# Optimization experiments

Measured on AMD Instinct MI355X. Metric: run time of the kernel, lower is better.

Reference implementation:

```python
import jax, jax.numpy as jnp
import numpy as np

B, M, D, H, FF = 2, 2048, 1024, 16, 2624
DH = D // H  # 64, power of 2 as required by the kernel
EPS = 1e-5
THETA = 10000.0


def setup_inputs() -> dict:
    key = jax.random.key(0)
    ks = jax.random.split(key, 12)
    hidden_states = jax.random.normal(ks[0], (B, M, D), dtype=jnp.float32)
    # padding mask: 1=valid, 0=pad; vary valid lengths per batch element
    lengths = jnp.array([M, 3 * M // 4], dtype=jnp.int32)
    attention_mask = (jnp.arange(M)[None, :] < lengths[:, None]).astype(jnp.int32)
    s = 0.02
    return {
        "hidden_states": hidden_states,
        "attention_mask": attention_mask,
        "ln1_w": jnp.ones((D,), jnp.float32),
        "ln1_b": jnp.zeros((D,), jnp.float32),
        "wqkv_w": s * jax.random.normal(ks[1], (3 * D, D), jnp.float32),
        "wqkv_b": jnp.zeros((3 * D,), jnp.float32),
        "wo_w": s * jax.random.normal(ks[2], (D, D), jnp.float32),
        "ln2_w": jnp.ones((D,), jnp.float32),
        "ln2_b": jnp.zeros((D,), jnp.float32),
        "wi_w": s * jax.random.normal(ks[3], (2 * FF, D), jnp.float32),
        "wo_mlp_w": s * jax.random.normal(ks[4], (D, FF), jnp.float32),
    }


def _layernorm(x, w, b):
    mu = jnp.mean(x, axis=-1, keepdims=True)
    var = jnp.mean(jnp.square(x - mu), axis=-1, keepdims=True)
    return (x - mu) * jax.lax.rsqrt(var + EPS) * w + b


def _rope(q, k):
    # q,k: [B,H,M,DH]; half-split RoPE (q1' = q1*c - q2*s; q2' = q1*s + q2*c)
    half = DH // 2
    inv_freq = 1.0 / (THETA ** (jnp.arange(0, DH, 2, dtype=jnp.float32) / DH))  # [half]
    freqs = jnp.arange(M, dtype=jnp.float32)[:, None] * inv_freq[None, :]      # [M, half]
    c = jnp.cos(freqs)[None, None]  # [1,1,M,half]
    s = jnp.sin(freqs)[None, None]
    q1, q2 = q[..., :half], q[..., half:]
    k1, k2 = k[..., :half], k[..., half:]
    q = jnp.concatenate([q1 * c - q2 * s, q1 * s + q2 * c], axis=-1)
    k = jnp.concatenate([k1 * c - k2 * s, k1 * s + k2 * c], axis=-1)
    return q, k


def reference(hidden_states, attention_mask, ln1_w, ln1_b, wqkv_w, wqkv_b,
              wo_w, ln2_w, ln2_b, wi_w, wo_mlp_w):
    x = hidden_states
    xn = _layernorm(x, ln1_w, ln1_b)
    qkv = (xn @ wqkv_w.T + wqkv_b).reshape(B, M, 3, H, DH)
    q, k, v = [jnp.transpose(qkv[:, :, i], (0, 2, 1, 3)) for i in range(3)]  # [B,H,M,DH]
    q, k = _rope(q, k)
    scale = 1.0 / np.sqrt(DH)
    scores = jnp.einsum("bhmd,bhnd->bhmn", q, k) * scale
    keep = (attention_mask > 0)[:, None, None, :]  # [B,1,1,M] key-padding mask
    scores = jnp.where(keep, scores, -jnp.inf)
    attn = jax.nn.softmax(scores, axis=-1)
    o = jnp.einsum("bhmn,bhnd->bhmd", attn, v)
    attn_out = jnp.transpose(o, (0, 2, 1, 3)).reshape(B, M, D)
    x = x + attn_out @ wo_w.T
    # ModernBERT GeGLU MLP
    h = _layernorm(x, ln2_w, ln2_b)
    g = h @ wi_w.T
    inp, gate = g[..., :FF], g[..., FF:]
    x = x + (jax.nn.gelu(inp, approximate=False) * gate) @ wo_mlp_w.T
    return x
```

## Files before the change

### kernel.cpp

```cpp
#include <hip/hip_runtime.h>
#include <hip/hip_bf16.h>
#include <math.h>

#define BB 2
#define MM 2048
#define DD 1024
#define HH 16
#define DHH 64
#define FF_ 2624
#define FFP 2688
#define TT (BB*MM)

typedef unsigned short u16;
typedef __attribute__((ext_vector_type(4))) unsigned short ushort4v;
typedef __attribute__((ext_vector_type(8))) short short8;
typedef __attribute__((ext_vector_type(4))) float floatx4;
typedef __attribute__((ext_vector_type(16))) float floatx16;

#define SCALE2 0.18033688011112043f

#define WAITVM(N) asm volatile("s_waitcnt vmcnt(" #N ")" ::: "memory")
#define CFENCE()  asm volatile("" ::: "memory")

__device__ __forceinline__ u16 f2bf(float f) {
    __hip_bfloat16 h = __float2bfloat16(f);
    return *(u16*)&h;
}
__device__ __forceinline__ float bf2f(u16 u) {
    __hip_bfloat16 h; *(u16*)&h = u;
    return __bfloat162float(h);
}
__device__ __forceinline__ float gelu_exact(float x) {
    return 0.5f * x * (1.0f + erff(x * 0.70710678118654752f));
}
__device__ __forceinline__ void gload_lds16(const void* g, void* l) {
    __builtin_amdgcn_global_load_lds(
        (const __attribute__((address_space(1))) unsigned int*)g,
        (__attribute__((address_space(3))) unsigned int*)l, 16, 0, 0);
}
__device__ __forceinline__ unsigned int cvt_pk_bf16(float a, float b) {
    unsigned int r;
    asm("v_cvt_pk_bf16_f32 %0, %1, %2" : "=v"(r) : "v"(a), "v"(b));
    return r;
}
__device__ __forceinline__ short8 pack8(float a0, float a1, float a2, float a3,
                                        float a4, float a5, float a6, float a7) {
    union { unsigned int u[4]; short8 s; } r;
    r.u[0] = cvt_pk_bf16(a0, a1); r.u[1] = cvt_pk_bf16(a2, a3);
    r.u[2] = cvt_pk_bf16(a4, a5); r.u[3] = cvt_pk_bf16(a6, a7);
    return r.s;
}

__device__ __forceinline__ int xcd_swizzle(int id, int nb) {
    if (nb & 7) return id;
    return (id & 7) * (nb >> 3) + (id >> 3);
}

__global__ void cvt_all(const float* __restrict__ wqkv, const float* __restrict__ wo,
                        const float* __restrict__ wi, const float* __restrict__ womlp,
                        u16* __restrict__ dqkv, u16* __restrict__ dwo,
                        u16* __restrict__ dinp, u16* __restrict__ dgate,
                        u16* __restrict__ dmlp, float2* __restrict__ tab) {
    int bid = blockIdx.x, tid = threadIdx.x;
    if (bid < 3072) {
        int i = (bid * 256 + tid) * 4;
        float4 v = *(const float4*)(wqkv + i);
        ushort4v o = {f2bf(v.x), f2bf(v.y), f2bf(v.z), f2bf(v.w)};
        *(ushort4v*)(dqkv + i) = o;
    } else if (bid < 4096) {
        int i = ((bid - 3072) * 256 + tid) * 4;
        float4 v = *(const float4*)(wo + i);
        ushort4v o = {f2bf(v.x), f2bf(v.y), f2bf(v.z), f2bf(v.w)};
        *(ushort4v*)(dwo + i) = o;
    } else if (bid < 4096 + 2 * FFP) {
        int seg = (bid - 4096) / FFP;
        int row = (bid - 4096) % FFP;
        u16* dst = seg ? dgate : dinp;
        const float* src = wi + (size_t)(seg ? FF_ : 0) * DD;
        int c = tid * 4;
        ushort4v o = {0, 0, 0, 0};
        if (row < FF_) {
            float4 v = *(const float4*)(src + (size_t)row * DD + c);
            o.x = f2bf(v.x); o.y = f2bf(v.y); o.z = f2bf(v.z); o.w = f2bf(v.w);
        }
        *(ushort4v*)(dst + (size_t)row * DD + c) = o;
    } else if (bid < 4096 + 2 * FFP + 1024) {
        int row = bid - 4096 - 2 * FFP;
        for (int c = tid * 4; c < FFP; c += 1024) {
            ushort4v o = {0, 0, 0, 0};
            if (c < FF_) {
                float4 v = *(const float4*)(womlp + (size_t)row * FF_ + c);
                o.x = f2bf(v.x); o.y = f2bf(v.y); o.z = f2bf(v.z); o.w = f2bf(v.w);
            }
            *(ushort4v*)(dmlp + (size_t)row * FFP + c) = o;
        }
    } else {
        int bq = bid - (4096 + 2 * FFP + 1024);
        int base = bq * 1024;
        for (int idx = tid; idx < 1024; idx += 256) {
            int e = base + idx;
            int mi = e >> 5, i = e & 31;
            float fr = (float)mi * powf(10000.0f, -(float)i / 32.0f);
            tab[e] = make_float2(cosf(fr), sinf(fr));
        }
    }
}

__global__ void ln_kernel(const float* __restrict__ x, const float* __restrict__ w,
                          const float* __restrict__ b, u16* __restrict__ out) {
    int row = blockIdx.x;
    int tid = threadIdx.x;
    const float4 v = ((const float4*)(x + (size_t)row * DD))[tid];
    float s  = v.x + v.y + v.z + v.w;
    float ss = v.x*v.x + v.y*v.y + v.z*v.z + v.w*v.w;
    #pragma unroll
    for (int o = 32; o > 0; o >>= 1) { s += __shfl_down(s, o); ss += __shfl_down(ss, o); }
    __shared__ float sbuf[4], ssbuf[4];
    int wid = tid >> 6;
    if ((tid & 63) == 0) { sbuf[wid] = s; ssbuf[wid] = ss; }
    __syncthreads();
    float st  = sbuf[0] + sbuf[1] + sbuf[2] + sbuf[3];
    float sst = ssbuf[0] + ssbuf[1] + ssbuf[2] + ssbuf[3];
    float mean = st * (1.0f / DD);
    float var  = sst * (1.0f / DD) - mean * mean;
    float rstd = rsqrtf(var + 1e-5f);
    const float4 wv = ((const float4*)w)[tid];
    const float4 bv = ((const float4*)b)[tid];
    ushort4v o;
    o.x = f2bf((v.x - mean) * rstd * wv.x + bv.x);
    o.y = f2bf((v.y - mean) * rstd * wv.y + bv.y);
    o.z = f2bf((v.z - mean) * rstd * wv.z + bv.z);
    o.w = f2bf((v.w - mean) * rstd * wv.w + bv.w);
    ((ushort4v*)(out + (size_t)row * DD))[tid] = o;
}


template<int MODE, bool OUT_BF16>
__global__ __launch_bounds__(256, 4)
void mfma_gemm64(const u16* __restrict__ A, const u16* __restrict__ W,
                 const float* __restrict__ bias, const void* __restrict__ add,
                 void* __restrict__ Cout, int N, int K) {
    __shared__ u16 As[3][128 * 32];
    __shared__ u16 Bs[3][64 * 32];
    int tid = threadIdx.x;
    int w = tid >> 6, lane = tid & 63;
    int q = lane >> 4, m = lane & 15;

    int nbx = gridDim.x;
    int id = xcd_swizzle(blockIdx.y * nbx + blockIdx.x, nbx * gridDim.y);
    int bx = id % nbx, by = id / nbx;
    int row0 = by * 128, col0 = bx * 64;
    int wm = (w >> 1) * 64, wn = (w & 1) * 32;

    floatx4 acc[4][2];
    #pragma unroll
    for (int i = 0; i < 4; i++)
        #pragma unroll
        for (int j = 0; j < 2; j++)
            acc[i][j] = (floatx4){0.f, 0.f, 0.f, 0.f};

    int lrow = lane >> 2;
    int lcg  = (lane & 3) ^ ((lrow >> 1) & 3);
    const u16* Ag = A + (size_t)(row0 + w * 32 + lrow) * K + lcg * 8;
    const u16* Bg = W + (size_t)(col0 + w * 16 + lrow) * K + lcg * 8;
    int NT = K >> 5;
    int slot8 = (q ^ ((m >> 1) & 3)) * 8;

    auto stage = [&](int t, int buf) {
        const u16* Aq = Ag + (size_t)t * 32;
        const u16* Bq = Bg + (size_t)t * 32;
        gload_lds16(Aq,                  &As[buf][(w * 32) * 32]);
        gload_lds16(Aq + (size_t)16 * K, &As[buf][(w * 32 + 16) * 32]);
        gload_lds16(Bq,                  &Bs[buf][(w * 16) * 32]);
    };
    stage(0, 0); stage(1, 1);

    int cur = 0;
    for (int t = 0; t < NT; ++t) {
        if (t + 2 < NT) {
            int nxt = cur + 2; if (nxt >= 3) nxt -= 3;
            stage(t + 2, nxt);
            WAITVM(6);
        } else if (t + 2 == NT) {
            WAITVM(3);
        } else {
            WAITVM(0);
        }
        __builtin_amdgcn_s_barrier();
        CFENCE();
        short8 af[4], bf[2];
        #pragma unroll
        for (int f = 0; f < 4; f++)
            af[f] = *(const short8*)&As[cur][(wm + f * 16 + m) * 32 + slot8];
        #pragma unroll
        for (int f = 0; f < 2; f++)
            bf[f] = *(const short8*)&Bs[cur][(wn + f * 16 + m) * 32 + slot8];
        __builtin_amdgcn_s_setprio(1);
        #pragma unroll
        for (int mf = 0; mf < 4; mf++)
            #pragma unroll
            for (int nf = 0; nf < 2; nf++)
                acc[mf][nf] = __builtin_amdgcn_mfma_f32_16x16x32_bf16(
                    af[mf], bf[nf], acc[mf][nf], 0, 0, 0);
        __builtin_amdgcn_s_setprio(0);
        if (t + 1 < NT) {
            __builtin_amdgcn_s_barrier();
            CFENCE();
        }
        cur = (cur + 1 == 3) ? 0 : cur + 1;
    }

    #pragma unroll
    for (int nf = 0; nf < 2; nf++) {
        int col = col0 + wn + nf * 16 + m;
        float bv = 0.f;
        if (MODE == 0 && bias) bv = bias[col];
        #pragma unroll
        for (int mf = 0; mf < 4; mf++) {
            #pragma unroll
            for (int r = 0; r < 4; r++) {
                int row = row0 + wm + mf * 16 + q * 4 + r;
                size_t idx = (size_t)row * N + col;
                float vacc = acc[mf][nf][r] + bv;
                if (MODE == 1) vacc += ((const float*)add)[idx];
                if (OUT_BF16) ((u16*)Cout)[idx] = f2bf(vacc);
                else          ((float*)Cout)[idx] = vacc;
            }
        }
    }
}

__global__ __launch_bounds__(256, 4)
void mfma_gemm_qkv(const u16* __restrict__ A, const u16* __restrict__ W,
                   const float* __restrict__ bias, const float2* __restrict__ tab,
                   u16* __restrict__ qb, u16* __restrict__ kb, u16* __restrict__ vtb) {
    __shared__ u16 As[3][128 * 32];
    __shared__ u16 Bs[3][64 * 32];
    int tid = threadIdx.x;
    int w = tid >> 6, lane = tid & 63;
    int q = lane >> 4, m = lane & 15;

    int nbx = gridDim.x;
    int id = xcd_swizzle(blockIdx.y * nbx + blockIdx.x, nbx * gridDim.y);
    int bx = id % nbx, by = id / nbx;
    int row0 = by * 128, col0 = bx * 64;
    int wm = w * 32;

    floatx4 acc[2][4];
    #pragma unroll
    for (int i = 0; i < 2; i++)
        #pragma unroll
        for (int j = 0; j < 4; j++)
            acc[i][j] = (floatx4){0.f, 0.f, 0.f, 0.f};

    int lrow = lane >> 2;
    int lcg  = (lane & 3) ^ ((lrow >> 1) & 3);
    const u16* Ag = A + (size_t)(row0 + w * 32 + lrow) * DD + lcg * 8;
    const u16* Bg = W + (size_t)(col0 + w * 16 + lrow) * DD + lcg * 8;
    const int NT = DD >> 5;
    int slot8 = (q ^ ((m >> 1) & 3)) * 8;

    auto stage = [&](int t, int buf) {
        const u16* Aq = Ag + (size_t)t * 32;
        const u16* Bq = Bg + (size_t)t * 32;
        gload_lds16(Aq,                   &As[buf][(w * 32) * 32]);
        gload_lds16(Aq + (size_t)16 * DD, &As[buf][(w * 32 + 16) * 32]);
        gload_lds16(Bq,                   &Bs[buf][(w * 16) * 32]);
    };
    stage(0, 0); stage(1, 1);

    int cur = 0;
    for (int t = 0; t < NT; ++t) {
        if (t + 2 < NT) {
            int nxt = cur + 2; if (nxt >= 3) nxt -= 3;
            stage(t + 2, nxt);
            WAITVM(6);
        } else if (t + 2 == NT) {
            WAITVM(3);
        } else {
            WAITVM(0);
        }
        __builtin_amdgcn_s_barrier();
        CFENCE();
        short8 af[2], bf[4];
        #pragma unroll
        for (int f = 0; f < 2; f++)
            af[f] = *(const short8*)&As[cur][(wm + f * 16 + m) * 32 + slot8];
        #pragma unroll
        for (int f = 0; f < 4; f++)
            bf[f] = *(const short8*)&Bs[cur][(f * 16 + m) * 32 + slot8];
        __builtin_amdgcn_s_setprio(1);
        #pragma unroll
        for (int mf = 0; mf < 2; mf++)
            #pragma unroll
            for (int nf = 0; nf < 4; nf++)
                acc[mf][nf] = __builtin_amdgcn_mfma_f32_16x16x32_bf16(
                    af[mf], bf[nf], acc[mf][nf], 0, 0, 0);
        __builtin_amdgcn_s_setprio(0);
        if (t + 1 < NT) {
            __builtin_amdgcn_s_barrier();
            CFENCE();
        }
        cur = (cur + 1 == 3) ? 0 : cur + 1;
    }

    int seg = col0 >> 6;
    int b   = row0 >> 11;
    int mi0 = (row0 & 2047) + wm;

    float b0[4];
    #pragma unroll
    for (int nf = 0; nf < 4; nf++) b0[nf] = bias[col0 + nf * 16 + m];

    if (seg < 32) {
        int hq = seg & 15;
        u16* dst = (seg < 16 ? qb : kb) + (size_t)(b * HH + hq) * MM * DHH;
        #pragma unroll
        for (int mf = 0; mf < 2; mf++) {
            #pragma unroll
            for (int r = 0; r < 4; r++) {
                int mi = mi0 + mf * 16 + q * 4 + r;
                float2 cs0 = tab[mi * 32 + m];
                float2 cs1 = tab[mi * 32 + 16 + m];
                float a0 = acc[mf][0][r] + b0[0];
                float a1 = acc[mf][1][r] + b0[1];
                float a2 = acc[mf][2][r] + b0[2];
                float a3 = acc[mf][3][r] + b0[3];
                size_t base = (size_t)mi * DHH;
                dst[base + m]      = f2bf(a0 * cs0.x - a2 * cs0.y);
                dst[base + 32 + m] = f2bf(a0 * cs0.y + a2 * cs0.x);
                dst[base + 16 + m] = f2bf(a1 * cs1.x - a3 * cs1.y);
                dst[base + 48 + m] = f2bf(a1 * cs1.y + a3 * cs1.x);
            }
        }
    } else {
        int hv = seg & 15;
        u16* dst = vtb + (size_t)(b * HH + hv) * DHH * MM;
        #pragma unroll
        for (int nf = 0; nf < 4; nf++) {
            int d = nf * 16 + m;
            #pragma unroll
            for (int mf = 0; mf < 2; mf++) {
                int mi = mi0 + mf * 16 + q * 4;
                ushort4v o;
                o.x = f2bf(acc[mf][nf][0] + b0[nf]);
                o.y = f2bf(acc[mf][nf][1] + b0[nf]);
                o.z = f2bf(acc[mf][nf][2] + b0[nf]);
                o.w = f2bf(acc[mf][nf][3] + b0[nf]);
                *(ushort4v*)(dst + (size_t)d * MM + mi) = o;
            }
        }
    }
}

__global__ __launch_bounds__(256, 3)
void mfma_gemm_glu(const u16* __restrict__ A, const u16* __restrict__ W1,
                   const u16* __restrict__ W2, u16* __restrict__ Cout) {
    __shared__ u16 As [3][128 * 32];
    __shared__ u16 B1s[3][64 * 32];
    __shared__ u16 B2s[3][64 * 32];
    int tid = threadIdx.x;
    int w = tid >> 6, lane = tid & 63;
    int q = lane >> 4, m = lane & 15;

    int nbx = gridDim.x;
    int id = xcd_swizzle(blockIdx.y * nbx + blockIdx.x, nbx * gridDim.y);
    int bx = id % nbx, by = id / nbx;
    int row0 = by * 128, col0 = bx * 64;
    int wm = (w >> 1) * 64, wn = (w & 1) * 32;

    floatx4 acc1[4][2], acc2[4][2];
    #pragma unroll
    for (int i = 0; i < 4; i++)
        #pragma unroll
        for (int j = 0; j < 2; j++) {
            acc1[i][j] = (floatx4){0.f, 0.f, 0.f, 0.f};
            acc2[i][j] = (floatx4){0.f, 0.f, 0.f, 0.f};
        }

    int lrow = lane >> 2;
    int lcg  = (lane & 3) ^ ((lrow >> 1) & 3);
    const u16* Ag  = A  + (size_t)(row0 + w * 32 + lrow) * DD + lcg * 8;
    const u16* B1g = W1 + (size_t)(col0 + w * 16 + lrow) * DD + lcg * 8;
    const u16* B2g = W2 + (size_t)(col0 + w * 16 + lrow) * DD + lcg * 8;
    const int NT = DD >> 5;
    int slot8 = (q ^ ((m >> 1) & 3)) * 8;

    auto stage = [&](int t, int buf) {
        const u16* Aq  = Ag  + (size_t)t * 32;
        const u16* B1q = B1g + (size_t)t * 32;
        const u16* B2q = B2g + (size_t)t * 32;
        gload_lds16(Aq,                   &As [buf][(w * 32) * 32]);
        gload_lds16(Aq + (size_t)16 * DD, &As [buf][(w * 32 + 16) * 32]);
        gload_lds16(B1q,                  &B1s[buf][(w * 16) * 32]);
        gload_lds16(B2q,                  &B2s[buf][(w * 16) * 32]);
    };
    stage(0, 0); stage(1, 1);

    int cur = 0;
    for (int t = 0; t < NT; ++t) {
        if (t + 2 < NT) {
            int nxt = cur + 2; if (nxt >= 3) nxt -= 3;
            stage(t + 2, nxt);
            WAITVM(8);
        } else if (t + 2 == NT) {
            WAITVM(4);
        } else {
            WAITVM(0);
        }
        __builtin_amdgcn_s_barrier();
        CFENCE();
        short8 af[4], b1f[2], b2f[2];
        #pragma unroll
        for (int f = 0; f < 4; f++)
            af[f] = *(const short8*)&As[cur][(wm + f * 16 + m) * 32 + slot8];
        #pragma unroll
        for (int f = 0; f < 2; f++) {
            b1f[f] = *(const short8*)&B1s[cur][(wn + f * 16 + m) * 32 + slot8];
            b2f[f] = *(const short8*)&B2s[cur][(wn + f * 16 + m) * 32 + slot8];
        }
        __builtin_amdgcn_s_setprio(1);
        #pragma unroll
        for (int mf = 0; mf < 4; mf++)
            #pragma unroll
            for (int nf = 0; nf < 2; nf++) {
                acc1[mf][nf] = __builtin_amdgcn_mfma_f32_16x16x32_bf16(
                    af[mf], b1f[nf], acc1[mf][nf], 0, 0, 0);
                acc2[mf][nf] = __builtin_amdgcn_mfma_f32_16x16x32_bf16(
                    af[mf], b2f[nf], acc2[mf][nf], 0, 0, 0);
            }
        __builtin_amdgcn_s_setprio(0);
        if (t + 1 < NT) {
            __builtin_amdgcn_s_barrier();
            CFENCE();
        }
        cur = (cur + 1 == 3) ? 0 : cur + 1;
    }

    #pragma unroll
    for (int nf = 0; nf < 2; nf++) {
        int col = col0 + wn + nf * 16 + m;
        #pragma unroll
        for (int mf = 0; mf < 4; mf++) {
            #pragma unroll
            for (int r = 0; r < 4; r++) {
                int row = row0 + wm + mf * 16 + q * 4 + r;
                Cout[(size_t)row * FFP + col] =
                    f2bf(gelu_exact(acc1[mf][nf][r]) * acc2[mf][nf][r]);
            }
        }
    }
}

__global__ __launch_bounds__(256, 2)
void flash_attn_mfma32(const u16* __restrict__ qp, const u16* __restrict__ kp,
                       const u16* __restrict__ vt, const int* __restrict__ mask,
                       u16* __restrict__ out) {
    __shared__ __align__(16) u16 Ks[2 * 64 * 64];
    __shared__ __align__(16) u16 Vs[2 * 64 * 64];

    int tid = threadIdx.x;
    int w = tid >> 6, lane = tid & 63;
    int col = lane & 31, hi = lane >> 5;
    int mt = blockIdx.x, h = blockIdx.y, b = blockIdx.z;
    int m0 = mt * 128;
    size_t bh = (size_t)(b * HH + h);
    const u16* qg  = qp + (bh * MM + m0 + w * 32) * DHH;
    const u16* kg  = kp + bh * MM * DHH;
    const u16* vtg = vt + bh * DHH * MM;

    int ntv = 0;
    for (int n = 0; n < MM; n += 64) ntv += (mask[b * MM + n] != 0);

    short8 qf[4];
    #pragma unroll
    for (int t = 0; t < 4; t++)
        qf[t] = *(const short8*)(qg + (size_t)col * DHH + (2 * t + hi) * 8);

    int lr = lane >> 3, lc = lane & 7;
    int lcg = lc ^ lr;
    int i0 = w * 16 + lr, i1 = i0 + 8;
    int sg0 = (i0 & ~12) | ((i0 & 4) << 1) | ((i0 & 8) >> 1);
    int sg1 = (i1 & ~12) | ((i1 & 4) << 1) | ((i1 & 8) >> 1);
    const u16* Kg0 = kg + (size_t)sg0 * DHH + lcg * 8;
    const u16* Kg1 = kg + (size_t)sg1 * DHH + lcg * 8;
    const u16* Vg0 = vtg + (size_t)i0 * MM + lcg * 8;
    const u16* Vg1 = vtg + (size_t)i1 * MM + lcg * 8;
    u16* KL0 = Ks + (w * 16) * 64;
    u16* KL1 = KL0 + 8 * 64;
    u16* VL0 = Vs + (w * 16) * 64;
    u16* VL1 = VL0 + 8 * 64;
    const int BUFO = 64 * 64;

    gload_lds16(Kg0, KL0); gload_lds16(Kg1, KL1);
    gload_lds16(Vg0, VL0); gload_lds16(Vg1, VL1);

    floatx16 O0, O1;
    #pragma unroll
    for (int r = 0; r < 16; r++) { O0[r] = 0.f; O1[r] = 0.f; }
    float ls = 0.f;

    int swz = (col & 7) * 8;

    for (int it = 0; it < ntv; ++it) {
        int cur = it & 1;
        int co = cur * BUFO, po = (cur ^ 1) * BUFO;
        if (it + 1 < ntv) {
            size_t nk = (size_t)(it + 1) * 64;
            gload_lds16(Kg0 + nk * DHH, KL0 + po);
            gload_lds16(Kg1 + nk * DHH, KL1 + po);
            gload_lds16(Vg0 + nk,       VL0 + po);
            gload_lds16(Vg1 + nk,       VL1 + po);
            WAITVM(4);
        } else {
            WAITVM(0);
        }
        __builtin_amdgcn_s_barrier();
        CFENCE();

        floatx16 P0, P1;
        #pragma unroll
        for (int r = 0; r < 16; r++) { P0[r] = 0.f; P1[r] = 0.f; }
        #pragma unroll
        for (int t = 0; t < 4; t++) {
            int ck = (((2 * t + hi) * 8) ^ swz);
            short8 kf0 = *(const short8*)&Ks[co + col * 64 + ck];
            short8 kf1 = *(const short8*)&Ks[co + (32 + col) * 64 + ck];
            __builtin_amdgcn_s_setprio(1);
            P0 = __builtin_amdgcn_mfma_f32_32x32x16_bf16(kf0, qf[t], P0, 0, 0, 0);
            P1 = __builtin_amdgcn_mfma_f32_32x32x16_bf16(kf1, qf[t], P1, 0, 0, 0);
            __builtin_amdgcn_s_setprio(0);
        }

        #pragma unroll
        for (int r = 0; r < 16; r++) {
            float e0 = exp2f(P0[r] * SCALE2);
            float e1 = exp2f(P1[r] * SCALE2);
            P0[r] = e0; P1[r] = e1;
            ls += e0 + e1;
        }

        short8 pa0 = pack8(P0[0], P0[1], P0[2],  P0[3],  P0[4],  P0[5],  P0[6],  P0[7]);
        short8 pa1 = pack8(P0[8], P0[9], P0[10], P0[11], P0[12], P0[13], P0[14], P0[15]);
        short8 pa2 = pack8(P1[0], P1[1], P1[2],  P1[3],  P1[4],  P1[5],  P1[6],  P1[7]);
        short8 pa3 = pack8(P1[8], P1[9], P1[10], P1[11], P1[12], P1[13], P1[14], P1[15]);

        #pragma unroll
        for (int s = 0; s < 4; s++) {
            int ck = (((2 * s + hi) * 8) ^ swz);
            short8 vf0 = *(const short8*)&Vs[co + col * 64 + ck];
            short8 vf1 = *(const short8*)&Vs[co + (32 + col) * 64 + ck];
            short8 pas = (s == 0) ? pa0 : (s == 1) ? pa1 : (s == 2) ? pa2 : pa3;
            __builtin_amdgcn_s_setprio(1);
            O0 = __builtin_amdgcn_mfma_f32_32x32x16_bf16(pas, vf0, O0, 0, 0, 0);
            O1 = __builtin_amdgcn_mfma_f32_32x32x16_bf16(pas, vf1, O1, 0, 0, 0);
            __builtin_amdgcn_s_setprio(0);
        }
        __builtin_amdgcn_s_barrier();
        CFENCE();
    }
    WAITVM(0);
    CFENCE();

    ls += __shfl_xor(ls, 32);
    float inv = 1.0f / ls;
    float invr[16];
    #pragma unroll
    for (int r = 0; r < 16; r++) {
        int crow = (r & 3) + 8 * (r >> 2) + 4 * hi;
        invr[r] = __shfl(inv, crow, 64);
    }
    u16* ob = out + ((size_t)(b * MM) + m0 + w * 32) * DD + h * DHH;
    #pragma unroll
    for (int r = 0; r < 16; r++) {
        int crow = (r & 3) + 8 * (r >> 2) + 4 * hi;
        ob[(size_t)crow * DD + col]      = f2bf(O0[r] * invr[r]);
        ob[(size_t)crow * DD + 32 + col] = f2bf(O1[r] * invr[r]);
    }
}

extern "C" void kernel_launch(void* const* d_in, const int* in_sizes, int n_in,
                              void* d_out, int out_size, void* d_ws, size_t ws_size,
                              hipStream_t stream) {
    const float* hidden   = (const float*)d_in[0];
    const int*   mask     = (const int*)d_in[1];
    const float* ln1_w    = (const float*)d_in[2];
    const float* ln1_b    = (const float*)d_in[3];
    const float* wqkv_w   = (const float*)d_in[4];
    const float* wqkv_b   = (const float*)d_in[5];
    const float* wo_w     = (const float*)d_in[6];
    const float* ln2_w    = (const float*)d_in[7];
    const float* ln2_b    = (const float*)d_in[8];
    const float* wi_w     = (const float*)d_in[9];
    const float* wo_mlp_w = (const float*)d_in[10];
    float* out = (float*)d_out;

    char* ws = (char*)d_ws;
    u16* wqkv_bf  = (u16*)(ws);
    u16* wo_bf    = (u16*)(ws + 6291456);
    u16* wi_inp   = (u16*)(ws + 8388608);
    u16* wi_gate  = (u16*)(ws + 13893632);
    u16* womlp_bf = (u16*)(ws + 19398656);
    u16* xn       = (u16*)(ws + 24903680);
    float2* rtab  = (float2*)(ws + 33292288);
    u16* qb       = (u16*)(ws + 58458112);
    u16* kb       = (u16*)(ws + 66846720);
    u16* vtb      = (u16*)(ws + 75235328);
    u16* attn_out = (u16*)(ws + 83623936);
    u16* hb       = (u16*)(ws + 92012544);
    u16* act      = (u16*)(ws + 58458112);

    cvt_all<<<4096 + 2 * FFP + 1024 + 64, 256, 0, stream>>>(
        wqkv_w, wo_w, wi_w, wo_mlp_w, wqkv_bf, wo_bf, wi_inp, wi_gate, womlp_bf, rtab);
    ln_kernel<<<TT, 256, 0, stream>>>(hidden, ln1_w, ln1_b, xn);
    mfma_gemm_qkv<<<dim3(3 * DD / 64, TT / 128), 256, 0, stream>>>(
        xn, wqkv_bf, wqkv_b, rtab, qb, kb, vtb);
    flash_attn_mfma32<<<dim3(MM / 128, HH, BB), 256, 0, stream>>>(
        qb, kb, vtb, mask, attn_out);
    mfma_gemm64<1, false><<<dim3(DD / 64, TT / 128), 256, 0, stream>>>(
        attn_out, wo_bf, nullptr, hidden, out, DD, DD);
    ln_kernel<<<TT, 256, 0, stream>>>(out, ln2_w, ln2_b, hb);
    mfma_gemm_glu<<<dim3(FFP / 64, TT / 128), 256, 0, stream>>>(
        hb, wi_inp, wi_gate, act);
    mfma_gemm64<1, false><<<dim3(DD / 64, TT / 128), 256, 0, stream>>>(
        act, womlp_bf, nullptr, out, out, DD, FFP);
}
```

Baseline: 361.9 us.

## Rewrite GLU GEMM to direct-register loads with 128x128 tiles

The GeGLU GEMM drops its LDS triple-buffered pipeline and loads A and both weight fragments straight from global memory into registers, double-buffered in registers. The output tile widens from 128x64 to 128x128, with each wave computing 64x64 for both the inp and gate halves. This removes LDS traffic and barriers and doubles per-block MFMA work. In exchange it uses far more registers (64 accumulators of 4 floats plus 24 short8 buffers), lowers occupancy, loses the cross-wave data sharing LDS provided, and depends on L2/cache for reuse. FFP/128 is 21 blocks in x.

```diff
diff --git a/kernel.cpp b/kernel.cpp
--- a/kernel.cpp
+++ b/kernel.cpp
@@ -353,12 +353,9 @@
     }
 }
 
-__global__ __launch_bounds__(256, 3)
+__global__ __launch_bounds__(256, 2)
 void mfma_gemm_glu(const u16* __restrict__ A, const u16* __restrict__ W1,
                    const u16* __restrict__ W2, u16* __restrict__ Cout) {
-    __shared__ u16 As [3][128 * 32];
-    __shared__ u16 B1s[3][64 * 32];
-    __shared__ u16 B2s[3][64 * 32];
     int tid = threadIdx.x;
     int w = tid >> 6, lane = tid & 63;
     int q = lane >> 4, m = lane & 15;
@@ -366,79 +363,61 @@
     int nbx = gridDim.x;
     int id = xcd_swizzle(blockIdx.y * nbx + blockIdx.x, nbx * gridDim.y);
     int bx = id % nbx, by = id / nbx;
-    int row0 = by * 128, col0 = bx * 64;
-    int wm = (w >> 1) * 64, wn = (w & 1) * 32;
-
-    floatx4 acc1[4][2], acc2[4][2];
+    int row0 = by * 128, col0 = bx * 128;
+    int wm = (w >> 1) * 64, wn = (w & 1) * 64;
+
+    floatx4 acc1[4][4], acc2[4][4];
     #pragma unroll
     for (int i = 0; i < 4; i++)
         #pragma unroll
-        for (int j = 0; j < 2; j++) {
+        for (int j = 0; j < 4; j++) {
             acc1[i][j] = (floatx4){0.f, 0.f, 0.f, 0.f};
             acc2[i][j] = (floatx4){0.f, 0.f, 0.f, 0.f};
         }
 
-    int lrow = lane >> 2;
-    int lcg  = (lane & 3) ^ ((lrow >> 1) & 3);
-    const u16* Ag  = A  + (size_t)(row0 + w * 32 + lrow) * DD + lcg * 8;
-    const u16* B1g = W1 + (size_t)(col0 + w * 16 + lrow) * DD + lcg * 8;
-    const u16* B2g = W2 + (size_t)(col0 + w * 16 + lrow) * DD + lcg * 8;
+    const u16* Ab  = A  + (size_t)(row0 + wm + m) * DD + q * 8;
+    const u16* B1b = W1 + (size_t)(col0 + wn + m) * DD + q * 8;
+    const u16* B2b = W2 + (size_t)(col0 + wn + m) * DD + q * 8;
+
+    short8 a[2][4], b1[2][4], b2[2][4];
+
+#define GLU_LOAD(S, T) do {                                                   \
+    _Pragma("unroll")                                                         \
+    for (int f = 0; f < 4; f++) {                                             \
+        a[S][f]  = *(const short8*)(Ab  + (size_t)f * 16 * DD + (T) * 32);    \
+        b1[S][f] = *(const short8*)(B1b + (size_t)f * 16 * DD + (T) * 32);    \
+        b2[S][f] = *(const short8*)(B2b + (size_t)f * 16 * DD + (T) * 32);    \
+    } } while (0)
+
+#define GLU_MFMA(S) do {                                                      \
+    __builtin_amdgcn_s_setprio(1);                                            \
+    _Pragma("unroll")                                                         \
+    for (int mf = 0; mf < 4; mf++)                                            \
+        _Pragma("unroll")                                                     \
+        for (int nf = 0; nf < 4; nf++) {                                      \
+            acc1[mf][nf] = __builtin_amdgcn_mfma_f32_16x16x32_bf16(           \
+                a[S][mf], b1[S][nf], acc1[mf][nf], 0, 0, 0);                  \
+            acc2[mf][nf] = __builtin_amdgcn_mfma_f32_16x16x32_bf16(           \
+                a[S][mf], b2[S][nf], acc2[mf][nf], 0, 0, 0);                  \
+        }                                                                     \
+    __builtin_amdgcn_s_setprio(0); } while (0)
+
     const int NT = DD >> 5;
-    int slot8 = (q ^ ((m >> 1) & 3)) * 8;
-
-    auto stage = [&](int t, int buf) {
-        const u16* Aq  = Ag  + (size_t)t * 32;
-        const u16* B1q = B1g + (size_t)t * 32;
-        const u16* B2q = B2g + (size_t)t * 32;
-        gload_lds16(Aq,                   &As [buf][(w * 32) * 32]);
-        gload_lds16(Aq + (size_t)16 * DD, &As [buf][(w * 32 + 16) * 32]);
-        gload_lds16(B1q,                  &B1s[buf][(w * 16) * 32]);
-        gload_lds16(B2q,                  &B2s[buf][(w * 16) * 32]);
-    };
-    stage(0, 0); stage(1, 1);
-
-    int cur = 0;
-    for (int t = 0; t < NT; ++t) {
-        if (t + 2 < NT) {
-            int nxt = cur + 2; if (nxt >= 3) nxt -= 3;
-            stage(t + 2, nxt);
-            WAITVM(8);
-        } else if (t + 2 == NT) {
-            WAITVM(4);
-        } else {
-            WAITVM(0);
-        }
-        __builtin_amdgcn_s_barrier();
-        CFENCE();
-        short8 af[4], b1f[2], b2f[2];
-        #pragma unroll
-        for (int f = 0; f < 4; f++)
-            af[f] = *(const short8*)&As[cur][(wm + f * 16 + m) * 32 + slot8];
-        #pragma unroll
-        for (int f = 0; f < 2; f++) {
-            b1f[f] = *(const short8*)&B1s[cur][(wn + f * 16 + m) * 32 + slot8];
-            b2f[f] = *(const short8*)&B2s[cur][(wn + f * 16 + m) * 32 + slot8];
-        }
-        __builtin_amdgcn_s_setprio(1);
-        #pragma unroll
-        for (int mf = 0; mf < 4; mf++)
-            #pragma unroll
-            for (int nf = 0; nf < 2; nf++) {
-                acc1[mf][nf] = __builtin_amdgcn_mfma_f32_16x16x32_bf16(
-                    af[mf], b1f[nf], acc1[mf][nf], 0, 0, 0);
-                acc2[mf][nf] = __builtin_amdgcn_mfma_f32_16x16x32_bf16(
-                    af[mf], b2f[nf], acc2[mf][nf], 0, 0, 0);
-            }
-        __builtin_amdgcn_s_setprio(0);
-        if (t + 1 < NT) {
-            __builtin_amdgcn_s_barrier();
-            CFENCE();
-        }
-        cur = (cur + 1 == 3) ? 0 : cur + 1;
-    }
-
-    #pragma unroll
-    for (int nf = 0; nf < 2; nf++) {
+    GLU_LOAD(0, 0);
+    for (int t = 0; t + 2 < NT; t += 2) {
+        GLU_LOAD(1, t + 1);
+        GLU_MFMA(0);
+        GLU_LOAD(0, t + 2);
+        GLU_MFMA(1);
+    }
+    GLU_LOAD(1, NT - 1);
+    GLU_MFMA(0);
+    GLU_MFMA(1);
+#undef GLU_LOAD
+#undef GLU_MFMA
+
+    #pragma unroll
+    for (int nf = 0; nf < 4; nf++) {
         int col = col0 + wn + nf * 16 + m;
         #pragma unroll
         for (int mf = 0; mf < 4; mf++) {
@@ -620,7 +599,7 @@
     mfma_gemm64<1, false><<<dim3(DD / 64, TT / 128), 256, 0, stream>>>(
         attn_out, wo_bf, nullptr, hidden, out, DD, DD);
     ln_kernel<<<TT, 256, 0, stream>>>(out, ln2_w, ln2_b, hb);
-    mfma_gemm_glu<<<dim3(FFP / 64, TT / 128), 256, 0, stream>>>(
+    mfma_gemm_glu<<<dim3(FFP / 128, TT / 128), 256, 0, stream>>>(
         hb, wi_inp, wi_gate, act);
     mfma_gemm64<1, false><<<dim3(DD / 64, TT / 128), 256, 0, stream>>>(
         act, womlp_bf, nullptr, out, out, DD, FFP);
```

Result: slower. 439.8 us (+21.5%).

## Deepen attention K/V pipeline to four LDS buffers, two tiles per barrier

Applied to the files above, without the earlier changes.

The flash-attention kernel's K/V staging grows from a double buffer to a four-slot ring in LDS. Each loop iteration now prefetches the next two 64-key tiles and computes two tiles between barriers. This is meant to halve the barrier count and keep more global loads in flight while the MFMAs run. In exchange, LDS per block doubles to 32 KB, which could lower occupancy, and the code gains tail handling for an odd tile count.

```diff
diff --git a/kernel.cpp b/kernel.cpp
--- a/kernel.cpp
+++ b/kernel.cpp
@@ -456,8 +456,8 @@
 void flash_attn_mfma32(const u16* __restrict__ qp, const u16* __restrict__ kp,
                        const u16* __restrict__ vt, const int* __restrict__ mask,
                        u16* __restrict__ out) {
-    __shared__ __align__(16) u16 Ks[2 * 64 * 64];
-    __shared__ __align__(16) u16 Vs[2 * 64 * 64];
+    __shared__ __align__(16) u16 Ks[4 * 64 * 64];
+    __shared__ __align__(16) u16 Vs[4 * 64 * 64];
 
     int tid = threadIdx.x;
     int w = tid >> 6, lane = tid & 63;
@@ -492,8 +492,14 @@
     u16* VL1 = VL0 + 8 * 64;
     const int BUFO = 64 * 64;
 
-    gload_lds16(Kg0, KL0); gload_lds16(Kg1, KL1);
-    gload_lds16(Vg0, VL0); gload_lds16(Vg1, VL1);
+    auto stage_tile = [&](int t, int buf) {
+        size_t nk = (size_t)t * 64;
+        int o = buf * BUFO;
+        gload_lds16(Kg0 + nk * DHH, KL0 + o);
+        gload_lds16(Kg1 + nk * DHH, KL1 + o);
+        gload_lds16(Vg0 + nk,       VL0 + o);
+        gload_lds16(Vg1 + nk,       VL1 + o);
+    };
 
     floatx16 O0, O1;
     #pragma unroll
@@ -502,22 +508,7 @@
 
     int swz = (col & 7) * 8;
 
-    for (int it = 0; it < ntv; ++it) {
-        int cur = it & 1;
-        int co = cur * BUFO, po = (cur ^ 1) * BUFO;
-        if (it + 1 < ntv) {
-            size_t nk = (size_t)(it + 1) * 64;
-            gload_lds16(Kg0 + nk * DHH, KL0 + po);
-            gload_lds16(Kg1 + nk * DHH, KL1 + po);
-            gload_lds16(Vg0 + nk,       VL0 + po);
-            gload_lds16(Vg1 + nk,       VL1 + po);
-            WAITVM(4);
-        } else {
-            WAITVM(0);
-        }
-        __builtin_amdgcn_s_barrier();
-        CFENCE();
-
+    auto compute_tile = [&](int co) {
         floatx16 P0, P1;
         #pragma unroll
         for (int r = 0; r < 16; r++) { P0[r] = 0.f; P1[r] = 0.f; }
@@ -531,7 +522,6 @@
             P1 = __builtin_amdgcn_mfma_f32_32x32x16_bf16(kf1, qf[t], P1, 0, 0, 0);
             __builtin_amdgcn_s_setprio(0);
         }
-
         #pragma unroll
         for (int r = 0; r < 16; r++) {
             float e0 = exp2f(P0[r] * SCALE2);
@@ -539,12 +529,10 @@
             P0[r] = e0; P1[r] = e1;
             ls += e0 + e1;
         }
-
         short8 pa0 = pack8(P0[0], P0[1], P0[2],  P0[3],  P0[4],  P0[5],  P0[6],  P0[7]);
         short8 pa1 = pack8(P0[8], P0[9], P0[10], P0[11], P0[12], P0[13], P0[14], P0[15]);
         short8 pa2 = pack8(P1[0], P1[1], P1[2],  P1[3],  P1[4],  P1[5],  P1[6],  P1[7]);
         short8 pa3 = pack8(P1[8], P1[9], P1[10], P1[11], P1[12], P1[13], P1[14], P1[15]);
-
         #pragma unroll
         for (int s = 0; s < 4; s++) {
             int ck = (((2 * s + hi) * 8) ^ swz);
@@ -556,8 +544,38 @@
             O1 = __builtin_amdgcn_mfma_f32_32x32x16_bf16(pas, vf1, O1, 0, 0, 0);
             __builtin_amdgcn_s_setprio(0);
         }
+    };
+
+    stage_tile(0, 0);
+    stage_tile(1, 1);
+
+    int base = 0;
+    for (; base + 1 < ntv; base += 2) {
+        int pre = ntv - (base + 2);
+        if (pre >= 2) {
+            stage_tile(base + 2, (base + 2) & 3);
+            stage_tile(base + 3, (base + 3) & 3);
+            WAITVM(8);
+        } else if (pre == 1) {
+            stage_tile(base + 2, (base + 2) & 3);
+            WAITVM(4);
+        } else {
+            WAITVM(0);
+        }
         __builtin_amdgcn_s_barrier();
         CFENCE();
+        compute_tile((base & 3) * BUFO);
+        compute_tile(((base + 1) & 3) * BUFO);
+        if (base + 3 < ntv) {
+            __builtin_amdgcn_s_barrier();
+            CFENCE();
+        }
+    }
+    if (base < ntv) {
+        WAITVM(0);
+        __builtin_amdgcn_s_barrier();
+        CFENCE();
+        compute_tile((base & 3) * BUFO);
     }
     WAITVM(0);
     CFENCE();
```

Result: no change. 360.7 us (-0.3%).
